# Optimization experiments

Hardware: AMD Instinct MI355X
Metric: run time of the kernel (lower is better)

The kernel has to match this reference:

```python
import jax, jax.numpy as jnp
import numpy as np

# ---- static config (matches init_kwargs) ----
B = 8            # batch_size (graphs)
N = 10000        # num_nodes per graph
NTOT = B * N     # total node rows (80000)
E = 320000       # edges (only over first N nodes, as in the original code)
D = 128          # input_dim == backbone_channels (shared conv forces equality)
H = 4            # heads
C = 128          # backbone_channels (per-head out dim, concat=False)
L = 3            # num_backbone_layers
K = 30           # sort-pool k
HID = 512        # mlp_hidden_dim
OUT = 2          # output_dim
EXPECTED = K * L * C * H + 1  # buggy mlp_input_dim from __init__ -> zero-pad
BN_EPS = 1e-5


def setup_inputs() -> dict:
    key = jax.random.key(0)
    ks = jax.random.split(key, 20)
    s = 1.0 / np.sqrt(D)
    inp = {
        "x": jax.random.normal(ks[0], (NTOT, D), dtype=jnp.float32),
        "edge_index": jax.random.randint(ks[1], (2, E), 0, N, dtype=jnp.int32),
        "age": jax.random.normal(ks[2], (B,), dtype=jnp.float32),
        # shared TransformerConv params (reused across all L layers)
        "Wq": jax.random.normal(ks[3], (D, H * C), dtype=jnp.float32) * s,
        "bq": jax.random.normal(ks[4], (H * C,), dtype=jnp.float32) * 0.02,
        "Wk": jax.random.normal(ks[5], (D, H * C), dtype=jnp.float32) * s,
        "bk": jax.random.normal(ks[6], (H * C,), dtype=jnp.float32) * 0.02,
        "Wv": jax.random.normal(ks[7], (D, H * C), dtype=jnp.float32) * s,
        "bv": jax.random.normal(ks[8], (H * C,), dtype=jnp.float32) * 0.02,
        "Wskip": jax.random.normal(ks[9], (D, C), dtype=jnp.float32) * s,
        "bskip": jax.random.normal(ks[10], (C,), dtype=jnp.float32) * 0.02,
        # per-layer BatchNorm (eval mode: running stats)
        "bn_gamma": 1.0 + 0.1 * jax.random.normal(ks[11], (L, C), dtype=jnp.float32),
        "bn_beta": 0.1 * jax.random.normal(ks[12], (L, C), dtype=jnp.float32),
        "bn_mean": 0.1 * jax.random.normal(ks[13], (L, C), dtype=jnp.float32),
        "bn_var": jax.random.uniform(ks[14], (L, C), dtype=jnp.float32, minval=0.5, maxval=1.5),
        # MLP head (2 layers: EXPECTED->HID, ReLU, HID->OUT)
        "W1": jax.random.normal(ks[15], (EXPECTED, HID), dtype=jnp.float32) * (1.0 / np.sqrt(EXPECTED)),
        "b1": jnp.zeros((HID,), dtype=jnp.float32),
        "W2": jax.random.normal(ks[16], (HID, OUT), dtype=jnp.float32) * (1.0 / np.sqrt(HID)),
        "b2": jnp.zeros((OUT,), dtype=jnp.float32),
    }
    return inp


def _transformer_conv(h, src, dst, Wq, bq, Wk, bk, Wv, bv, Wskip, bskip):
    # PyG TransformerConv, concat=False, root_weight=True, eval (no attn dropout)
    q = (h @ Wq + bq).reshape(NTOT, H, C)
    k = (h @ Wk + bk).reshape(NTOT, H, C)
    v = (h @ Wv + bv).reshape(NTOT, H, C)
    # per-edge attention logits [E, H]
    alpha = jnp.einsum("ehc,ehc->eh", q[dst], k[src]) / np.sqrt(C).astype(np.float32)
    # segment softmax over incoming edges of each target node
    m = jax.ops.segment_max(alpha, dst, num_segments=NTOT)          # [NTOT, H]
    e = jnp.exp(alpha - m[dst])
    denom = jax.ops.segment_sum(e, dst, num_segments=NTOT)          # [NTOT, H]
    a = e / (denom[dst] + 1e-16)                                    # [E, H]
    out = jax.ops.segment_sum(a[:, :, None] * v[src], dst, num_segments=NTOT)  # [NTOT,H,C]
    return out.mean(axis=1) + h @ Wskip + bskip                     # concat=False -> head mean


def reference(x, edge_index, age, Wq, bq, Wk, bk, Wv, bv, Wskip, bskip,
              bn_gamma, bn_beta, bn_mean, bn_var, W1, b1, W2, b2):
    src, dst = edge_index[0], edge_index[1]
    h = x
    feats = []
    for i in range(L):  # fixed small layer count; shared conv weights
        h = _transformer_conv(h, src, dst, Wq, bq, Wk, bk, Wv, bv, Wskip, bskip)
        h = (h - bn_mean[i]) * (bn_gamma[i] / jnp.sqrt(bn_var[i] + BN_EPS)) + bn_beta[i]
        h = jax.nn.relu(h)  # dropout: eval mode no-op
        feats.append(h)
    h = feats[-1]  # concat_input_graph=False
    # global_sort_pool: sort nodes per graph by last channel (desc), take top-k
    xr = h.reshape(B, N, C)
    idx = jnp.argsort(-xr[:, :, -1], axis=1)[:, :K]                 # [B, K]
    pooled = jnp.take_along_axis(xr, idx[:, :, None], axis=1)       # [B, K, C]
    z = pooled.reshape(B, K * C)
    z = jnp.concatenate([z, age.reshape(B, 1)], axis=1)             # [B, K*C+1]
    # zero-pad to the (mismatched) expected MLP input dim, as in the original
    z = jnp.concatenate([z, jnp.zeros((B, EXPECTED - z.shape[1]), dtype=z.dtype)], axis=1)
    z = jax.nn.relu(z @ W1 + b1)
    z = z @ W2 + b2
    return jax.nn.log_softmax(z, axis=-1)
```

## Files before the change

### kernel.cpp

```cpp
#include <hip/hip_runtime.h>
#include <cmath>


#define NN    10000
#define NTOT  80000
#define EE    320000
#define CH    128

__device__ __forceinline__ float rl_f(float v, int lane) {
    return __uint_as_float(__builtin_amdgcn_readlane(__float_as_uint(v), lane));
}

__global__ __launch_bounds__(256) void precompute_kernel(
    const float* __restrict__ Wq, const float* __restrict__ bq,
    const float* __restrict__ Wk, const float* __restrict__ Wv,
    const float* __restrict__ bv, const float* __restrict__ Wskip,
    const float* __restrict__ bskip,
    const float* __restrict__ bn_gamma, const float* __restrict__ bn_beta,
    const float* __restrict__ bn_mean, const float* __restrict__ bn_var,
    float* __restrict__ Bcat, float* __restrict__ biascat,
    float* __restrict__ Wcomb, float* __restrict__ bvbar,
    float* __restrict__ bnS, float* __restrict__ bnB)
{
    const float inv_sqrtC = 0.08838834764831845f;
    int idx = blockIdx.x * 256 + threadIdx.x;
    if (idx < 65536) {
        int c = idx >> 9;
        int o = idx & 511;
        int hbase = o & ~127;
        int j = o & 127;
        const float* wq = Wq + c * 512 + hbase;
        const float* wk = Wk + j * 512 + hbase;
        float s = 0.f;
        for (int cc = 0; cc < 128; cc++) s = fmaf(wq[cc], wk[cc], s);
        Bcat[c * 640 + o] = s * inv_sqrtC;
        return;
    }
    idx -= 65536;
    if (idx < 16384) {
        int c = idx >> 7, n = idx & 127;
        Bcat[c * 640 + 512 + n] = Wskip[c * 128 + n];
        return;
    }
    idx -= 16384;
    if (idx < 512) {
        int o = idx, hbase = o & ~127, j = o & 127;
        const float* wk = Wk + j * 512 + hbase;
        const float* bqp = bq + hbase;
        float s = 0.f;
        for (int cc = 0; cc < 128; cc++) s = fmaf(bqp[cc], wk[cc], s);
        biascat[o] = s * inv_sqrtC;
        return;
    }
    idx -= 512;
    if (idx < 128) {
        biascat[512 + idx] = bskip[idx];
        return;
    }
    idx -= 128;
    if (idx < 65536) {
        int k = idx >> 7;
        int n = idx & 127;
        int h = k >> 7, c = k & 127;
        Wcomb[k * 128 + n] = Wv[c * 512 + h * 128 + n] * 0.25f;
        return;
    }
    idx -= 65536;
    if (idx < 128) {
        float s = 0.f;
        for (int h = 0; h < 4; h++) s += bv[h * 128 + idx];
        bvbar[idx] = 0.25f * s;
        return;
    }
    idx -= 128;
    if (idx < 384) {
        float sc = bn_gamma[idx] / sqrtf(bn_var[idx] + 1e-5f);
        bnS[idx] = sc;
        bnB[idx] = bn_beta[idx] - bn_mean[idx] * sc;
        return;
    }
}

__global__ void count_kernel(const int* __restrict__ dst, int* __restrict__ deg) {
    int e = blockIdx.x * 256 + threadIdx.x;
    if (e < EE) atomicAdd(&deg[dst[e]], 1);
}

__global__ __launch_bounds__(1024) void scan_kernel(const int* __restrict__ deg,
                                                    int* __restrict__ rowstart) {
    __shared__ int part[1024];
    const int t = threadIdx.x;
    int loc[10];
    int s = 0;
    for (int i = 0; i < 10; i++) {
        int idx = t * 10 + i;
        int v = (idx < NN) ? deg[idx] : 0;
        loc[i] = s; s += v;
    }
    part[t] = s; __syncthreads();
    for (int d = 1; d < 1024; d <<= 1) {
        int v = (t >= d) ? part[t - d] : 0;
        __syncthreads();
        part[t] += v;
        __syncthreads();
    }
    int base = (t == 0) ? 0 : part[t - 1];
    for (int i = 0; i < 10; i++) {
        int idx = t * 10 + i;
        if (idx <= NN) rowstart[idx] = base + loc[i];
    }
}

__global__ void scatter_kernel(const int* __restrict__ src, const int* __restrict__ dst,
                               const int* __restrict__ rowstart, int* __restrict__ cursor,
                               int* __restrict__ csr_src) {
    int e = blockIdx.x * 256 + threadIdx.x;
    if (e < EE) {
        int d = dst[e];
        int p = atomicAdd(&cursor[d], 1);
        csr_src[rowstart[d] + p] = src[e];
    }
}

__global__ __launch_bounds__(256) void skip2_keys_kernel(
    const float* __restrict__ xup,
    const float* __restrict__ Wskip,
    const float* __restrict__ bskip,
    const float* __restrict__ bnS, const float* __restrict__ bnB,
    float* __restrict__ h2up,
    float* __restrict__ gkeys)
{
    __shared__ float rowb[64][132];
    __shared__ float Bs[16][132];
    __shared__ float sWc[128];
    const int t = threadIdx.x;
    const int r0 = blockIdx.x * 64;
    const int Mrem = min(64, (NTOT - NN) - r0);
    const int tx = t & 15;
    const int ty = t >> 4;

    for (int f = t; f < 64 * 32; f += 256) {
        int row = f >> 5, c4 = (f & 31) * 4;
        if (row < Mrem)
            *(float4*)&rowb[row][c4] = *(const float4*)(xup + (size_t)(r0 + row) * CH + c4);
    }
    if (t < 128) sWc[t] = Wskip[t * 128 + 127];

    for (int l = 0; l < 2; l++) {
        float acc[4][8];
        #pragma unroll
        for (int i = 0; i < 4; i++)
            #pragma unroll
            for (int j = 0; j < 8; j++) acc[i][j] = 0.f;

        for (int k0 = 0; k0 < 128; k0 += 16) {
            __syncthreads();
            for (int f = t; f < 512; f += 256) {
                int kk = f >> 5, n4 = (f & 31) * 4;
                *(float4*)&Bs[kk][n4] = *(const float4*)(Wskip + (size_t)(k0 + kk) * 128 + n4);
            }
            __syncthreads();
            #pragma unroll
            for (int kk = 0; kk < 16; kk++) {
                const float4 b0 = *(const float4*)&Bs[kk][tx * 4];
                const float4 b1 = *(const float4*)&Bs[kk][64 + tx * 4];
                const float bf[8] = {b0.x, b0.y, b0.z, b0.w, b1.x, b1.y, b1.z, b1.w};
                #pragma unroll
                for (int i = 0; i < 4; i++) {
                    const float af = rowb[ty * 4 + i][k0 + kk];
                    #pragma unroll
                    for (int j = 0; j < 8; j++)
                        acc[i][j] = fmaf(af, bf[j], acc[i][j]);
                }
            }
        }
        __syncthreads();
        const float* bS = bnS + l * 128;
        const float* bB = bnB + l * 128;
        #pragma unroll
        for (int i = 0; i < 4; i++) {
            const int row = ty * 4 + i;
            float4 v0, v1;
            float* p0 = &v0.x;
            float* p1 = &v1.x;
            #pragma unroll
            for (int q = 0; q < 4; q++) {
                const int n0c = tx * 4 + q;
                float xv = acc[i][q] + bskip[n0c];
                xv = fmaf(xv, bS[n0c], bB[n0c]);
                p0[q] = fmaxf(xv, 0.f);
                const int n1c = 64 + tx * 4 + q;
                float yv = acc[i][4 + q] + bskip[n1c];
                yv = fmaf(yv, bS[n1c], bB[n1c]);
                p1[q] = fmaxf(yv, 0.f);
            }
            *(float4*)&rowb[row][tx * 4] = v0;
            *(float4*)&rowb[row][64 + tx * 4] = v1;
        }
    }
    __syncthreads();
    if (t < Mrem) {
        float s = 0.f;
        for (int k = 0; k < 128; k++) s = fmaf(rowb[t][k], sWc[k], s);
        s += bskip[127];
        s = fmaf(s, bnS[2 * 128 + 127], bnB[2 * 128 + 127]);
        gkeys[NN + r0 + t] = fmaxf(s, 0.f);
    }
    for (int f = t; f < 64 * 32; f += 256) {
        int row = f >> 5, c4 = (f & 31) * 4;
        if (row < Mrem)
            *(float4*)(h2up + (size_t)(r0 + row) * CH + c4) = *(const float4*)&rowb[row][c4];
    }
}

template<int BM, int BN, int TM, int TN, int MODE>
__global__ __launch_bounds__(256) void gemm_fp32(
    const float* __restrict__ A, int lda,
    const float* __restrict__ B, int ldb,
    const float* __restrict__ bias, const float* __restrict__ bias2,
    const int* __restrict__ deg,
    const float* __restrict__ Cold,
    const float* __restrict__ bnS, const float* __restrict__ bnB,
    float* __restrict__ C0, int ldc0,
    float* __restrict__ C1, int ldc1,
    int M, int K,
    float* __restrict__ keysOut)
{
    constexpr int BK = 16;
    __shared__ float As[BK][BM + 4];
    __shared__ float Bs[BK][BN + 4];
    const int t  = threadIdx.x;
    const int tx = t % (BN / TN);
    const int ty = t / (BN / TN);
    const int m0 = blockIdx.x * BM;
    const int n0 = blockIdx.y * BN;
    float acc[TM][TN];
    #pragma unroll
    for (int i = 0; i < TM; i++)
        #pragma unroll
        for (int j = 0; j < TN; j++) acc[i][j] = 0.f;

    for (int k0 = 0; k0 < K; k0 += BK) {
        #pragma unroll
        for (int f = t; f < BM * 4; f += 256) {
            int row = f >> 2, fc = f & 3;
            int gm = m0 + row;
            float4 v = make_float4(0.f, 0.f, 0.f, 0.f);
            if (gm < M) v = *(const float4*)(A + (size_t)gm * lda + k0 + fc * 4);
            As[fc * 4 + 0][row] = v.x;
            As[fc * 4 + 1][row] = v.y;
            As[fc * 4 + 2][row] = v.z;
            As[fc * 4 + 3][row] = v.w;
        }
        #pragma unroll
        for (int f = t; f < BK * (BN / 4); f += 256) {
            int kk = f / (BN / 4);
            int nn = (f % (BN / 4)) * 4;
            *(float4*)(&Bs[kk][nn]) = *(const float4*)(B + (size_t)(k0 + kk) * ldb + n0 + nn);
        }
        __syncthreads();
        #pragma unroll
        for (int kk = 0; kk < BK; kk++) {
            float af[TM], bf[TN];
            if constexpr (TM == 2) {
                float2 v = *(const float2*)&As[kk][ty * 2];
                af[0] = v.x; af[1] = v.y;
            } else {
                #pragma unroll
                for (int ii = 0; ii < TM; ii += 4) {
                    float4 v = *(const float4*)&As[kk][ty * TM + ii];
                    af[ii + 0] = v.x; af[ii + 1] = v.y; af[ii + 2] = v.z; af[ii + 3] = v.w;
                }
            }
            #pragma unroll
            for (int jj = 0; jj < TN; jj += 4) {
                float4 v = *(const float4*)&Bs[kk][tx * TN + jj];
                bf[jj + 0] = v.x; bf[jj + 1] = v.y; bf[jj + 2] = v.z; bf[jj + 3] = v.w;
            }
            #pragma unroll
            for (int i = 0; i < TM; i++)
                #pragma unroll
                for (int j = 0; j < TN; j++)
                    acc[i][j] = fmaf(af[i], bf[j], acc[i][j]);
        }
        __syncthreads();
    }
    #pragma unroll
    for (int i = 0; i < TM; i++) {
        int gm = m0 + ty * TM + i;
        if (gm >= M) continue;
        const bool addB2 = (MODE == 4) ? (deg[gm] > 0) : false;
        #pragma unroll
        for (int j = 0; j < TN; j += 4) {
            const int nb = n0 + tx * TN + j;
            float4 v;
            float* vp = &v.x;
            if (MODE == 4) {
                const float4 old = *(const float4*)(Cold + (size_t)gm * ldc1 + nb);
                const float* op = &old.x;
                #pragma unroll
                for (int q = 0; q < 4; q++) {
                    const int n = nb + q;
                    float x = acc[i][j + q] + op[q];
                    if (addB2) x += bias2[n];
                    x = fmaf(x, bnS[n], bnB[n]);
                    vp[q] = fmaxf(x, 0.f);
                }
                *(float4*)(C0 + (size_t)gm * ldc0 + nb) = v;
                if (keysOut != nullptr && nb == 124) keysOut[gm] = v.w;
            } else {
                #pragma unroll
                for (int q = 0; q < 4; q++)
                    vp[q] = acc[i][j + q] + bias[nb + q];
                if (nb < 512)
                    *(float4*)(C0 + (size_t)gm * ldc0 + nb) = v;
                else
                    *(float4*)(C1 + (size_t)gm * ldc1 + nb - 512) = v;
            }
        }
    }
}

__global__ __launch_bounds__(256) void attn_kernel(
    const float* __restrict__ h,
    const float* __restrict__ u,
    float* __restrict__ g,
    const int* __restrict__ rowstart,
    const int* __restrict__ csr_src)
{
    __shared__ float h_lds[128 * 65];
    __shared__ __align__(16) float palpha[4 * 64 * 4];
    __shared__ __align__(16) float wT[64 * 4];
    __shared__ __align__(16) float scale_lds[4];
    __shared__ __align__(16) float s_lds[4];
    __shared__ __align__(16) float merge[128 * 4];
    __shared__ int src_lds[64];

    const int n  = blockIdx.x;
    const int t  = threadIdx.x;
    const int w  = t >> 6;
    const int l  = t & 63;
    const int c  = t & 127;
    const int jh = t >> 7;
    const int rs   = rowstart[n];
    const int degn = rowstart[n + 1] - rs;

    if (degn == 0) {
        g[(size_t)n * 512 + t] = 0.f;
        g[(size_t)n * 512 + 256 + t] = 0.f;
        return;
    }
    float u_reg0 = u[(size_t)n * 512 + ((l >> 5)) * 128 + 32 * w + (l & 31)];
    float u_reg1 = u[(size_t)n * 512 + ((l >> 5) + 2) * 128 + 32 * w + (l & 31)];

    float m_run = -INFINITY, s_run = 0.f;
    float4 acc4 = make_float4(0.f, 0.f, 0.f, 0.f);

    for (int base = 0; base < degn; base += 64) {
        const int len = min(64, degn - base);
        __syncthreads();
        if (t < len) src_lds[t] = csr_src[rs + base + t];
        __syncthreads();
        for (int f = t; f < len * 32; f += 256) {
            const int j = f >> 5, c4 = (f & 31) * 4;
            const float4 v = *(const float4*)(h + (size_t)src_lds[j] * CH + c4);
            h_lds[(c4 + 0) * 65 + j] = v.x;
            h_lds[(c4 + 1) * 65 + j] = v.y;
            h_lds[(c4 + 2) * 65 + j] = v.z;
            h_lds[(c4 + 3) * 65 + j] = v.w;
        }
        __syncthreads();
        {
            float p0 = 0.f, p1 = 0.f, p2 = 0.f, p3 = 0.f;
            #pragma unroll
            for (int dc = 0; dc < 32; dc++) {
                const float hv = h_lds[(32 * w + dc) * 65 + l];
                p0 = fmaf(rl_f(u_reg0, dc),      hv, p0);
                p1 = fmaf(rl_f(u_reg0, 32 + dc), hv, p1);
                p2 = fmaf(rl_f(u_reg1, dc),      hv, p2);
                p3 = fmaf(rl_f(u_reg1, 32 + dc), hv, p3);
            }
            palpha[(0 * 64 + l) * 4 + w] = p0;
            palpha[(1 * 64 + l) * 4 + w] = p1;
            palpha[(2 * 64 + l) * 4 + w] = p2;
            palpha[(3 * 64 + l) * 4 + w] = p3;
        }
        __syncthreads();
        {
            const float4 pa = *(const float4*)&palpha[(w * 64 + l) * 4];
            float alpha = (l < len) ? (pa.x + pa.y + pa.z + pa.w) : -INFINITY;
            float mx = alpha;
            #pragma unroll
            for (int d = 1; d < 64; d <<= 1) mx = fmaxf(mx, __shfl_xor(mx, d, 64));
            const float newm = fmaxf(m_run, mx);
            float e = (l < len) ? __expf(alpha - newm) : 0.f;
            float ss = e;
            #pragma unroll
            for (int d = 1; d < 64; d <<= 1) ss += __shfl_xor(ss, d, 64);
            const float sc = (m_run == -INFINITY) ? 0.f : __expf(m_run - newm);
            s_run = s_run * sc + ss;
            m_run = newm;
            wT[l * 4 + w] = e;
            if (l == 0) scale_lds[w] = sc;
        }
        __syncthreads();
        {
            const float4 scv = *(const float4*)scale_lds;
            acc4.x *= scv.x; acc4.y *= scv.y; acc4.z *= scv.z; acc4.w *= scv.w;
            const int j0 = jh * 32;
            const int j1 = min(len, j0 + 32);
            for (int j = j0; j < j1; j++) {
                const float hv = h_lds[c * 65 + j];
                const float4 wv = *(const float4*)&wT[j * 4];
                acc4.x = fmaf(wv.x, hv, acc4.x);
                acc4.y = fmaf(wv.y, hv, acc4.y);
                acc4.z = fmaf(wv.z, hv, acc4.z);
                acc4.w = fmaf(wv.w, hv, acc4.w);
            }
        }
    }
    if (l == 0) s_lds[w] = s_run;
    __syncthreads();
    if (jh == 1) *(float4*)&merge[c * 4] = acc4;
    __syncthreads();
    if (jh == 0) {
        const float4 o  = *(const float4*)&merge[c * 4];
        const float4 sv = *(const float4*)s_lds;
        g[(size_t)n * 512 + 0 * 128 + c] = (acc4.x + o.x) / (sv.x + 1e-16f);
        g[(size_t)n * 512 + 1 * 128 + c] = (acc4.y + o.y) / (sv.y + 1e-16f);
        g[(size_t)n * 512 + 2 * 128 + c] = (acc4.z + o.z) / (sv.z + 1e-16f);
        g[(size_t)n * 512 + 3 * 128 + c] = (acc4.w + o.w) / (sv.w + 1e-16f);
    }
}

__global__ __launch_bounds__(256) void radix_pool_kernel(
    const float* __restrict__ gkeys, const float* __restrict__ age,
    int* __restrict__ sel, float* __restrict__ z)
{
    __shared__ unsigned int keys[NN];
    __shared__ int hist[256];
    __shared__ int sbuf[256];
    __shared__ unsigned int sel_prefix;
    __shared__ int sel_need;
    __shared__ int gt_counter;
    __shared__ unsigned int cand_key[30];
    __shared__ int cand_idx[30];
    __shared__ int order[30];

    const int b = blockIdx.x;
    const int t = threadIdx.x;

    for (int i = t; i < NN; i += 256)
        keys[i] = __float_as_uint(gkeys[(size_t)b * NN + i]);
    if (t == 0) { sel_prefix = 0u; sel_need = 30; gt_counter = 0; }
    __syncthreads();

    for (int r = 3; r >= 0; r--) {
        hist[t] = 0;
        __syncthreads();
        const int shift = r * 8;
        const unsigned int pmask = (r == 3) ? 0u : (0xFFFFFFFFu << ((r + 1) * 8));
        const unsigned int pref = sel_prefix;
        const int need = sel_need;
        for (int i = t; i < NN; i += 256) {
            unsigned int k = keys[i];
            if ((k & pmask) == pref)
                atomicAdd(&hist[(k >> shift) & 255u], 1);
        }
        __syncthreads();
        sbuf[t] = hist[255 - t];
        __syncthreads();
        for (int d = 1; d < 256; d <<= 1) {
            int o = (t >= d) ? sbuf[t - d] : 0;
            __syncthreads();
            sbuf[t] += o;
            __syncthreads();
        }
        {
            const int v = t;
            const int ge = sbuf[255 - v];
            const int gt = ge - hist[v];
            if (gt < need && need <= ge) {
                sel_prefix = pref | ((unsigned int)v << shift);
                sel_need = need - gt;
            }
        }
        __syncthreads();
    }

    const unsigned int T = sel_prefix;
    const int need_eq = sel_need;
    const int n_gt = 30 - need_eq;

    for (int i = t; i < NN; i += 256) {
        unsigned int k = keys[i];
        if (k > T) {
            int p = atomicAdd(&gt_counter, 1);
            cand_key[p] = k; cand_idx[p] = i;
        }
    }
    {
        const int CHK = (NN + 255) / 256;
        const int i0 = t * CHK, i1 = min(NN, i0 + CHK);
        int local = 0;
        for (int i = i0; i < i1; i++) if (keys[i] == T) local++;
        sbuf[t] = local;
        __syncthreads();
        for (int d = 1; d < 256; d <<= 1) {
            int o = (t >= d) ? sbuf[t - d] : 0;
            __syncthreads();
            sbuf[t] += o;
            __syncthreads();
        }
        int rank = (t == 0) ? 0 : sbuf[t - 1];
        for (int i = i0; i < i1; i++) {
            if (keys[i] == T) {
                if (rank < need_eq) { cand_key[n_gt + rank] = T; cand_idx[n_gt + rank] = i; }
                rank++;
            }
        }
    }
    __syncthreads();
    if (t < 30) {
        const unsigned int mk = cand_key[t];
        const int mi = cand_idx[t];
        int rk = 0;
        for (int j = 0; j < 30; j++) {
            const unsigned int ok = cand_key[j];
            const int oi = cand_idx[j];
            if (ok > mk || (ok == mk && oi < mi)) rk++;
        }
        order[rk] = t;
    }
    __syncthreads();
    if (t < 30) sel[b * 30 + t] = cand_idx[order[t]];
    if (t == 0) z[(size_t)b * 3841 + 3840] = age[b];
}

__global__ __launch_bounds__(128) void gather_kernel(
    const float* __restrict__ h3,
    const float* __restrict__ h2up,
    const float* __restrict__ Wskip, const float* __restrict__ bskip,
    const float* __restrict__ bnS, const float* __restrict__ bnB,
    const int* __restrict__ sel, float* __restrict__ z)
{
    __shared__ float sh[128];
    const int blk = blockIdx.x;
    const int b = blk / 30;
    const int kk = blk % 30;
    const int c = threadIdx.x;
    const int i = sel[b * 30 + kk];
    const size_t g = (size_t)b * NN + i;
    float v;
    if (b == 0) {
        v = h3[g * CH + c];
    } else {
        sh[c] = h2up[(g - NN) * CH + c];
        __syncthreads();
        float s = 0.f;
        for (int k = 0; k < 128; k++) s = fmaf(sh[k], Wskip[k * 128 + c], s);
        s += bskip[c];
        s = fmaf(s, bnS[2 * 128 + c], bnB[2 * 128 + c]);
        v = fmaxf(s, 0.f);
    }
    z[(size_t)b * 3841 + kk * CH + c] = v;
}

__global__ __launch_bounds__(256) void mlp1_kernel(
    const float* __restrict__ z, const float* __restrict__ W1,
    float* __restrict__ zh)
{
    __shared__ float zs[256];
    const int b  = blockIdx.x >> 4;
    const int ic = blockIdx.x & 15;
    const int t  = threadIdx.x;
    const int i0 = ic * 241;
    const int i1 = min(3841, i0 + 241);
    float a0 = 0.f, a1 = 0.f;
    for (int cb = i0; cb < i1; cb += 256) {
        int cl = min(256, i1 - cb);
        __syncthreads();
        if (t < cl) zs[t] = z[(size_t)b * 3841 + cb + t];
        __syncthreads();
        #pragma unroll 4
        for (int q = 0; q < cl; q++) {
            float zv = zs[q];
            const float* wp = W1 + (size_t)(cb + q) * 512;
            a0 = fmaf(zv, wp[t], a0);
            a1 = fmaf(zv, wp[t + 256], a1);
        }
    }
    atomicAdd(&zh[(size_t)b * 512 + t], a0);
    atomicAdd(&zh[(size_t)b * 512 + t + 256], a1);
}

__global__ __launch_bounds__(256) void mlp2_kernel(
    const float* __restrict__ zh, const float* __restrict__ b1,
    const float* __restrict__ W2, const float* __restrict__ b2,
    float* __restrict__ out)
{
    __shared__ float r0[256], r1[256];
    const int b = blockIdx.x;
    const int t = threadIdx.x;
    float a0 = 0.f, a1 = 0.f;
    for (int j = t; j < 512; j += 256) {
        float v = fmaxf(zh[(size_t)b * 512 + j] + b1[j], 0.f);
        a0 = fmaf(v, W2[j * 2 + 0], a0);
        a1 = fmaf(v, W2[j * 2 + 1], a1);
    }
    r0[t] = a0; r1[t] = a1; __syncthreads();
    for (int s = 128; s > 0; s >>= 1) {
        if (t < s) { r0[t] += r0[t + s]; r1[t] += r1[t + s]; }
        __syncthreads();
    }
    if (t == 0) {
        float l0 = r0[0] + b2[0], l1 = r1[0] + b2[1];
        float m = fmaxf(l0, l1);
        float lse = m + logf(__expf(l0 - m) + __expf(l1 - m));
        out[b * 2 + 0] = l0 - lse;
        out[b * 2 + 1] = l1 - lse;
    }
}

extern "C" void kernel_launch(void* const* d_in, const int* in_sizes, int n_in,
                              void* d_out, int out_size, void* d_ws, size_t ws_size,
                              hipStream_t stream) {
    const float* x     = (const float*)d_in[0];
    const int*   ei    = (const int*)d_in[1];
    const float* age   = (const float*)d_in[2];
    const float* Wq    = (const float*)d_in[3];
    const float* bq    = (const float*)d_in[4];
    const float* Wk    = (const float*)d_in[5];
    const float* Wv    = (const float*)d_in[7];
    const float* bv    = (const float*)d_in[8];
    const float* Wskip = (const float*)d_in[9];
    const float* bskip = (const float*)d_in[10];
    const float* bn_g  = (const float*)d_in[11];
    const float* bn_b  = (const float*)d_in[12];
    const float* bn_m  = (const float*)d_in[13];
    const float* bn_v  = (const float*)d_in[14];
    const float* W1    = (const float*)d_in[15];
    const float* b1    = (const float*)d_in[16];
    const float* W2    = (const float*)d_in[17];
    const float* b2    = (const float*)d_in[18];

    float* ws = (float*)d_ws;
    float* h3      = ws;
    float* hlowA   = h3 + 10240000;
    float* hlowB   = hlowA + 1280000;
    float* u       = hlowB + 1280000;
    float* skipraw = u + 5120000;
    float* Bcat    = skipraw + 1280000;
    float* biascat = Bcat + 81920;
    float* Wcomb   = biascat + 640;
    float* bvbar   = Wcomb + 65536;
    float* bnS     = bvbar + 128;
    float* bnB     = bnS + 384;
    float* zbuf    = bnB + 384;
    float* zh      = zbuf + 30728;
    int* deg      = (int*)(zh + 4096);
    int* cursor   = deg + NN;
    int* rowstart = cursor + NN;
    int* csr_src  = rowstart + NN + 1;
    float* keysG  = (float*)(csr_src + EE);
    int* sel      = (int*)(keysG + NTOT);

    const int* srcI = ei;
    const int* dstI = ei + EE;

    hipMemsetAsync(deg, 0, sizeof(int) * (2 * NN), stream);
    hipMemsetAsync(zh, 0, sizeof(float) * 4096, stream);

    precompute_kernel<<<581, 256, 0, stream>>>(Wq, bq, Wk, Wv, bv, Wskip, bskip,
                                               bn_g, bn_b, bn_m, bn_v,
                                               Bcat, biascat, Wcomb, bvbar, bnS, bnB);
    count_kernel<<<1250, 256, 0, stream>>>(dstI, deg);
    scan_kernel<<<1, 1024, 0, stream>>>(deg, rowstart);
    scatter_kernel<<<1250, 256, 0, stream>>>(srcI, dstI, rowstart, cursor, csr_src);

    skip2_keys_kernel<<<1094, 256, 0, stream>>>(x + (size_t)NN * CH, Wskip, bskip,
                                                bnS, bnB, h3 + (size_t)NN * CH, keysG);

    const float* hcur = x;
    for (int l = 0; l < 3; l++) {
        float* dest = (l == 0) ? hlowA : (l == 1) ? hlowB : h3;
        gemm_fp32<64, 64, 4, 4, 0><<<dim3(157, 10), 256, 0, stream>>>(
            hcur, CH, Bcat, 640, biascat, nullptr, nullptr, nullptr,
            nullptr, nullptr, u, 512, skipraw, CH, NN, 128, nullptr);
        attn_kernel<<<NN, 256, 0, stream>>>(hcur, u, u, rowstart, csr_src);
        gemm_fp32<32, 64, 2, 4, 4><<<dim3(313, 2), 256, 0, stream>>>(
            u, 512, Wcomb, CH, nullptr, bvbar, deg, skipraw,
            bnS + l * 128, bnB + l * 128, dest, CH, nullptr, CH, NN, 512,
            (l == 2) ? keysG : nullptr);
        hcur = dest;
    }
    radix_pool_kernel<<<8, 256, 0, stream>>>(keysG, age, sel, zbuf);
    gather_kernel<<<240, 128, 0, stream>>>(h3, h3 + (size_t)NN * CH, Wskip, bskip,
                                           bnS, bnB, sel, zbuf);
    mlp1_kernel<<<128, 256, 0, stream>>>(zbuf, W1, zh);
    mlp2_kernel<<<8, 256, 0, stream>>>(zh, b1, W2, b2, (float*)d_out);
}
```

Before: 623.0 us.

## Enlarge GEMM tiles, drop h2 store, recompute layers in gather for selected rows

The skip/keys kernel for graphs 1..7 now processes 128-row tiles with an 8x8 per-thread micro-tile and stops writing the layer-2 hidden state back to global memory. The gather kernel instead recomputes all three skip layers from x, only for the 30 selected rows per graph. The projection GEMM moves from 64x64/4x4 tiles to 128x128/8x8 tiles with split float4 fragment loads. This cuts global write traffic and improves register-level reuse. The costs are more register pressure, fewer blocks in flight, and a little extra compute in gather.

Result: slower. 653.8 us (+4.9%).

```diff
diff --git a/kernel.cpp b/kernel.cpp
--- a/kernel.cpp
+++ b/kernel.cpp
@@ -122,24 +122,23 @@
     }
 }
 
-__global__ __launch_bounds__(256) void skip2_keys_kernel(
+__global__ __launch_bounds__(256, 2) void skip_keys_kernel(
     const float* __restrict__ xup,
     const float* __restrict__ Wskip,
     const float* __restrict__ bskip,
     const float* __restrict__ bnS, const float* __restrict__ bnB,
-    float* __restrict__ h2up,
     float* __restrict__ gkeys)
 {
-    __shared__ float rowb[64][132];
+    __shared__ float rowb[128][132];
     __shared__ float Bs[16][132];
     __shared__ float sWc[128];
     const int t = threadIdx.x;
-    const int r0 = blockIdx.x * 64;
-    const int Mrem = min(64, (NTOT - NN) - r0);
+    const int r0 = blockIdx.x * 128;
+    const int Mrem = min(128, (NTOT - NN) - r0);
     const int tx = t & 15;
     const int ty = t >> 4;
 
-    for (int f = t; f < 64 * 32; f += 256) {
+    for (int f = t; f < 128 * 32; f += 256) {
         int row = f >> 5, c4 = (f & 31) * 4;
         if (row < Mrem)
             *(float4*)&rowb[row][c4] = *(const float4*)(xup + (size_t)(r0 + row) * CH + c4);
@@ -147,9 +146,9 @@
     if (t < 128) sWc[t] = Wskip[t * 128 + 127];
 
     for (int l = 0; l < 2; l++) {
-        float acc[4][8];
+        float acc[8][8];
         #pragma unroll
-        for (int i = 0; i < 4; i++)
+        for (int i = 0; i < 8; i++)
             #pragma unroll
             for (int j = 0; j < 8; j++) acc[i][j] = 0.f;
 
@@ -161,16 +160,32 @@
             }
             __syncthreads();
             #pragma unroll
-            for (int kk = 0; kk < 16; kk++) {
-                const float4 b0 = *(const float4*)&Bs[kk][tx * 4];
-                const float4 b1 = *(const float4*)&Bs[kk][64 + tx * 4];
-                const float bf[8] = {b0.x, b0.y, b0.z, b0.w, b1.x, b1.y, b1.z, b1.w};
+            for (int kq = 0; kq < 4; kq++) {
+                float4 a4[8];
                 #pragma unroll
-                for (int i = 0; i < 4; i++) {
-                    const float af = rowb[ty * 4 + i][k0 + kk];
+                for (int i = 0; i < 8; i++)
+                    a4[i] = *(const float4*)&rowb[ty + 16 * i][k0 + kq * 4];
+                float4 c0[4], c1[4];
+                #pragma unroll
+                for (int q = 0; q < 4; q++) {
+                    c0[q] = *(const float4*)&Bs[kq * 4 + q][tx * 4];
+                    c1[q] = *(const float4*)&Bs[kq * 4 + q][64 + tx * 4];
+                }
+                #pragma unroll
+                for (int q = 0; q < 4; q++) {
                     #pragma unroll
-                    for (int j = 0; j < 8; j++)
-                        acc[i][j] = fmaf(af, bf[j], acc[i][j]);
+                    for (int i = 0; i < 8; i++) {
+                        const float av = (q == 0) ? a4[i].x : (q == 1) ? a4[i].y
+                                       : (q == 2) ? a4[i].z : a4[i].w;
+                        acc[i][0] = fmaf(av, c0[q].x, acc[i][0]);
+                        acc[i][1] = fmaf(av, c0[q].y, acc[i][1]);
+                        acc[i][2] = fmaf(av, c0[q].z, acc[i][2]);
+                        acc[i][3] = fmaf(av, c0[q].w, acc[i][3]);
+                        acc[i][4] = fmaf(av, c1[q].x, acc[i][4]);
+                        acc[i][5] = fmaf(av, c1[q].y, acc[i][5]);
+                        acc[i][6] = fmaf(av, c1[q].z, acc[i][6]);
+                        acc[i][7] = fmaf(av, c1[q].w, acc[i][7]);
+                    }
                 }
             }
         }
@@ -178,8 +193,8 @@
         const float* bS = bnS + l * 128;
         const float* bB = bnB + l * 128;
         #pragma unroll
-        for (int i = 0; i < 4; i++) {
-            const int row = ty * 4 + i;
+        for (int i = 0; i < 8; i++) {
+            const int row = ty + 16 * i;
             float4 v0, v1;
             float* p0 = &v0.x;
             float* p1 = &v1.x;
@@ -205,11 +220,6 @@
         s += bskip[127];
         s = fmaf(s, bnS[2 * 128 + 127], bnB[2 * 128 + 127]);
         gkeys[NN + r0 + t] = fmaxf(s, 0.f);
-    }
-    for (int f = t; f < 64 * 32; f += 256) {
-        int row = f >> 5, c4 = (f & 31) * 4;
-        if (row < Mrem)
-            *(float4*)(h2up + (size_t)(r0 + row) * CH + c4) = *(const float4*)&rowb[row][c4];
     }
 }
 
@@ -265,17 +275,23 @@
             if constexpr (TM == 2) {
                 float2 v = *(const float2*)&As[kk][ty * 2];
                 af[0] = v.x; af[1] = v.y;
+            } else if constexpr (TM == 4) {
+                float4 v = *(const float4*)&As[kk][ty * 4];
+                af[0] = v.x; af[1] = v.y; af[2] = v.z; af[3] = v.w;
             } else {
-                #pragma unroll
-                for (int ii = 0; ii < TM; ii += 4) {
-                    float4 v = *(const float4*)&As[kk][ty * TM + ii];
-                    af[ii + 0] = v.x; af[ii + 1] = v.y; af[ii + 2] = v.z; af[ii + 3] = v.w;
-                }
-            }
-            #pragma unroll
-            for (int jj = 0; jj < TN; jj += 4) {
-                float4 v = *(const float4*)&Bs[kk][tx * TN + jj];
-                bf[jj + 0] = v.x; bf[jj + 1] = v.y; bf[jj + 2] = v.z; bf[jj + 3] = v.w;
+                float4 v = *(const float4*)&As[kk][ty * 4];
+                float4 w = *(const float4*)&As[kk][BM / 2 + ty * 4];
+                af[0] = v.x; af[1] = v.y; af[2] = v.z; af[3] = v.w;
+                af[4] = w.x; af[5] = w.y; af[6] = w.z; af[7] = w.w;
+            }
+            if constexpr (TN == 4) {
+                float4 v = *(const float4*)&Bs[kk][tx * 4];
+                bf[0] = v.x; bf[1] = v.y; bf[2] = v.z; bf[3] = v.w;
+            } else {
+                float4 v = *(const float4*)&Bs[kk][tx * 4];
+                float4 w = *(const float4*)&Bs[kk][BN / 2 + tx * 4];
+                bf[0] = v.x; bf[1] = v.y; bf[2] = v.z; bf[3] = v.w;
+                bf[4] = w.x; bf[5] = w.y; bf[6] = w.z; bf[7] = w.w;
             }
             #pragma unroll
             for (int i = 0; i < TM; i++)
@@ -287,12 +303,13 @@
     }
     #pragma unroll
     for (int i = 0; i < TM; i++) {
-        int gm = m0 + ty * TM + i;
+        const int gm = m0 + ((TM == 8) ? ((i < 4) ? ty * 4 + i : BM / 2 + ty * 4 + (i - 4))
+                                       : ty * TM + i);
         if (gm >= M) continue;
         const bool addB2 = (MODE == 4) ? (deg[gm] > 0) : false;
         #pragma unroll
-        for (int j = 0; j < TN; j += 4) {
-            const int nb = n0 + tx * TN + j;
+        for (int h = 0; h < TN / 4; h++) {
+            const int nb = n0 + ((TN == 8) ? h * (BN / 2) + tx * 4 : tx * TN + h * 4);
             float4 v;
             float* vp = &v.x;
             if (MODE == 4) {
@@ -301,7 +318,7 @@
                 #pragma unroll
                 for (int q = 0; q < 4; q++) {
                     const int n = nb + q;
-                    float x = acc[i][j + q] + op[q];
+                    float x = acc[i][h * 4 + q] + op[q];
                     if (addB2) x += bias2[n];
                     x = fmaf(x, bnS[n], bnB[n]);
                     vp[q] = fmaxf(x, 0.f);
@@ -311,7 +328,7 @@
             } else {
                 #pragma unroll
                 for (int q = 0; q < 4; q++)
-                    vp[q] = acc[i][j + q] + bias[nb + q];
+                    vp[q] = acc[i][h * 4 + q] + bias[nb + q];
                 if (nb < 512)
                     *(float4*)(C0 + (size_t)gm * ldc0 + nb) = v;
                 else
@@ -539,12 +556,12 @@
 
 __global__ __launch_bounds__(128) void gather_kernel(
     const float* __restrict__ h3,
-    const float* __restrict__ h2up,
+    const float* __restrict__ x,
     const float* __restrict__ Wskip, const float* __restrict__ bskip,
     const float* __restrict__ bnS, const float* __restrict__ bnB,
     const int* __restrict__ sel, float* __restrict__ z)
 {
-    __shared__ float sh[128];
+    __shared__ float buf0[128], buf1[128];
     const int blk = blockIdx.x;
     const int b = blk / 30;
     const int kk = blk % 30;
@@ -555,13 +572,24 @@
     if (b == 0) {
         v = h3[g * CH + c];
     } else {
-        sh[c] = h2up[(g - NN) * CH + c];
+        float* rd = buf0;
+        float* wr = buf1;
+        buf0[c] = x[g * CH + c];
         __syncthreads();
         float s = 0.f;
-        for (int k = 0; k < 128; k++) s = fmaf(sh[k], Wskip[k * 128 + c], s);
-        s += bskip[c];
-        s = fmaf(s, bnS[2 * 128 + c], bnB[2 * 128 + c]);
-        v = fmaxf(s, 0.f);
+        for (int l = 0; l < 3; l++) {
+            s = 0.f;
+            for (int k = 0; k < 128; k++) s = fmaf(rd[k], Wskip[k * 128 + c], s);
+            s += bskip[c];
+            s = fmaf(s, bnS[l * 128 + c], bnB[l * 128 + c]);
+            s = fmaxf(s, 0.f);
+            if (l < 2) {
+                wr[c] = s;
+                __syncthreads();
+                float* tmp = rd; rd = wr; wr = tmp;
+            }
+        }
+        v = s;
     }
     z[(size_t)b * 3841 + kk * CH + c] = v;
 }
@@ -678,13 +706,13 @@
     scan_kernel<<<1, 1024, 0, stream>>>(deg, rowstart);
     scatter_kernel<<<1250, 256, 0, stream>>>(srcI, dstI, rowstart, cursor, csr_src);
 
-    skip2_keys_kernel<<<1094, 256, 0, stream>>>(x + (size_t)NN * CH, Wskip, bskip,
-                                                bnS, bnB, h3 + (size_t)NN * CH, keysG);
+    skip_keys_kernel<<<547, 256, 0, stream>>>(x + (size_t)NN * CH, Wskip, bskip,
+                                              bnS, bnB, keysG);
 
     const float* hcur = x;
     for (int l = 0; l < 3; l++) {
         float* dest = (l == 0) ? hlowA : (l == 1) ? hlowB : h3;
-        gemm_fp32<64, 64, 4, 4, 0><<<dim3(157, 10), 256, 0, stream>>>(
+        gemm_fp32<128, 128, 8, 8, 0><<<dim3(79, 5), 256, 0, stream>>>(
             hcur, CH, Bcat, 640, biascat, nullptr, nullptr, nullptr,
             nullptr, nullptr, u, 512, skipraw, CH, NN, 128, nullptr);
         attn_kernel<<<NN, 256, 0, stream>>>(hcur, u, u, rowstart, csr_src);
@@ -695,7 +723,7 @@
         hcur = dest;
     }
     radix_pool_kernel<<<8, 256, 0, stream>>>(keysG, age, sel, zbuf);
-    gather_kernel<<<240, 128, 0, stream>>>(h3, h3 + (size_t)NN * CH, Wskip, bskip,
+    gather_kernel<<<240, 128, 0, stream>>>(h3, x, Wskip, bskip,
                                            bnS, bnB, sel, zbuf);
     mlp1_kernel<<<128, 256, 0, stream>>>(zbuf, W1, zh);
     mlp2_kernel<<<8, 256, 0, stream>>>(zh, b1, W2, b2, (float*)d_out);
```
